# Kernel tuning notes

Measured on AMD Instinct MI355X. Metric: run time of the kernel, lower is better.

The kernel has to match this reference:

```python
import jax, jax.numpy as jnp
import numpy as np

B, T, F, H = 8, 1024, 512, 8
DK = F // H
P = 2 * T - 1  # relative position length


def setup_inputs() -> dict:
    key = jax.random.key(0)
    ks = jax.random.split(key, 16)
    s = 0.02
    inp = {
        "query": jax.random.normal(ks[0], (B, T, F), jnp.float32),
        "key": jax.random.normal(ks[1], (B, T, F), jnp.float32),
        "value": jax.random.normal(ks[2], (B, T, F), jnp.float32),
        "mask": jax.random.randint(ks[3], (B, T, T), 0, 2) > 0,
        "pos_emb": jax.random.normal(ks[4], (1, P, F), jnp.float32),
        "Wq": jax.random.normal(ks[5], (F, F), jnp.float32) * s,
        "bq": jnp.zeros((F,), jnp.float32),
        "Wk": jax.random.normal(ks[6], (F, F), jnp.float32) * s,
        "bk": jnp.zeros((F,), jnp.float32),
        "Wv": jax.random.normal(ks[7], (F, F), jnp.float32) * s,
        "bv": jnp.zeros((F,), jnp.float32),
        "Wpos": jax.random.normal(ks[8], (F, F), jnp.float32) * s,
        "Wo": jax.random.normal(ks[9], (F, F), jnp.float32) * s,
        "bo": jnp.zeros((F,), jnp.float32),
        "pos_bias_u": jax.random.normal(ks[10], (H, DK), jnp.float32) * s,
        "pos_bias_v": jax.random.normal(ks[11], (H, DK), jnp.float32) * s,
    }
    return inp


def _rel_shift(x):
    # x: (b, h, q, p) with p = 2q-1 ; Transformer-XL pad/reshape/slice trick
    b, h, q, p = x.shape
    x = jnp.pad(x, ((0, 0), (0, 0), (0, 0), (1, 0)))
    x = x.reshape(b, h, p + 1, q)[:, :, 1:, :].reshape(b, h, q, p)
    return x


def reference(query, key, value, mask, pos_emb, Wq, bq, Wk, bk, Wv, bv,
              Wpos, Wo, bo, pos_bias_u, pos_bias_v):
    b = query.shape[0]
    # projections (torch Linear: y = x @ W.T + b), split into heads -> (b,h,t,d)
    q = (query @ Wq.T + bq).reshape(b, -1, H, DK).transpose(0, 2, 1, 3)
    k = (key @ Wk.T + bk).reshape(b, -1, H, DK).transpose(0, 2, 1, 3)
    v = (value @ Wv.T + bv).reshape(b, -1, H, DK).transpose(0, 2, 1, 3)
    # positional projection: (1,P,F) -> (h,P,d)
    p = (pos_emb @ Wpos.T).reshape(-1, H, DK).transpose(1, 0, 2)

    q_u = q + pos_bias_u[None, :, None, :]
    q_v = q + pos_bias_v[None, :, None, :]

    matrix_ac = jnp.einsum("bhqd,bhkd->bhqk", q_u, k)
    matrix_bd = jnp.einsum("bhqd,hpd->bhqp", q_v, p)
    matrix_bd = _rel_shift(matrix_bd)[:, :, :, : matrix_ac.shape[-1]]

    scores = (matrix_ac + matrix_bd) / jnp.sqrt(jnp.float32(DK))
    m = mask[:, None, :, :]
    scores = jnp.where(m, -10000.0, scores)
    attn = jax.nn.softmax(scores, axis=-1)
    attn = jnp.where(m, 0.0, attn)

    x = jnp.einsum("bhqk,bhkd->bhqd", attn, v)
    x = x.transpose(0, 2, 1, 3).reshape(b, -1, H * DK)
    return x @ Wo.T + bo
```

## Files before the change

kernel.cpp:

```cpp
#include <hip/hip_runtime.h>

#define Bn 8
#define Tn 1024
#define Fn 512
#define Hn 8
#define DKn 64
#define Pn 2047

namespace {

typedef _Float16 h8 __attribute__((ext_vector_type(8)));
typedef float f4 __attribute__((ext_vector_type(4)));

__device__ __forceinline__ unsigned short f2h(float f) {
  _Float16 h = (_Float16)f;
  return __builtin_bit_cast(unsigned short, h);
}

__device__ __forceinline__ f4 mfma16(h8 a, h8 b, f4 c) {
  return __builtin_amdgcn_mfma_f32_16x16x32_f16(a, b, c, 0, 0, 0);
}

__device__ __forceinline__ h8 frag_ld(const unsigned char* p, int row, int kk, int grp) {
  int off = row * 128 + kk * 64 + grp * 16;
  off ^= (row & 7) << 4;
  return *(const h8*)(p + off);
}

__global__ void detect_kernel(const unsigned int* m, int* flag) {
  if (threadIdx.x == 0) {
    int bm = 0;
    for (int i = 0; i < 256; ++i)
      if (m[i] > 1u) bm = 1;
    *flag = bm;
  }
}

template <int MODE>
__global__ __launch_bounds__(256) void proj_kernel(
    const float* __restrict__ Af, const unsigned short* __restrict__ Ah,
    const float* __restrict__ W, const float* __restrict__ bias,
    const float* __restrict__ pbu, const float* __restrict__ pbv,
    unsigned short* __restrict__ o0, unsigned short* __restrict__ o1,
    float* __restrict__ ofp, int M) {
  __shared__ __align__(16) unsigned char sA[64 * 128];
  __shared__ __align__(16) unsigned char sB[64 * 128];

  const int t = threadIdx.x;
  const int w = t >> 6, l = t & 63;
  const int grp = l >> 4, lc = l & 15;
  const int m0 = blockIdx.x * 64, n0 = blockIdx.y * 64;
  const int srow = t >> 2, sseg = t & 3;

  f4 acc[4];
#pragma unroll
  for (int c = 0; c < 4; ++c) acc[c] = {0.f, 0.f, 0.f, 0.f};

  for (int kt = 0; kt < 8; ++kt) {
    {
      int gm = m0 + srow;
      int sw = (srow & 7) << 4;
      if (MODE == 4) {
        const unsigned short* ar = Ah + (size_t)gm * Fn + kt * 64 + sseg * 16;
#pragma unroll
        for (int hh = 0; hh < 2; ++hh) {
          uint4 qd = *(const uint4*)(ar + hh * 8);
          int off = srow * 128 + sseg * 32 + hh * 16;
          *(uint2*)(sA + ((off) ^ sw)) = make_uint2(qd.x, qd.y);
          *(uint2*)(sA + ((off + 8) ^ sw)) = make_uint2(qd.z, qd.w);
        }
      } else {
        bool valid = (gm < M);
        const float* ar = Af + (size_t)gm * Fn + kt * 64 + sseg * 16;
#pragma unroll
        for (int i = 0; i < 4; ++i) {
          float4 fv = valid ? *(const float4*)(ar + 4 * i) : make_float4(0.f, 0.f, 0.f, 0.f);
          uint2 pk;
          pk.x = (unsigned)f2h(fv.x) | ((unsigned)f2h(fv.y) << 16);
          pk.y = (unsigned)f2h(fv.z) | ((unsigned)f2h(fv.w) << 16);
          int off = srow * 128 + sseg * 32 + i * 8;
          *(uint2*)(sA + (off ^ sw)) = pk;
        }
      }
      const float* br = W + (size_t)(n0 + srow) * Fn + kt * 64 + sseg * 16;
#pragma unroll
      for (int i = 0; i < 4; ++i) {
        float4 fv = *(const float4*)(br + 4 * i);
        uint2 pk;
        pk.x = (unsigned)f2h(fv.x) | ((unsigned)f2h(fv.y) << 16);
        pk.y = (unsigned)f2h(fv.z) | ((unsigned)f2h(fv.w) << 16);
        int off = srow * 128 + sseg * 32 + i * 8;
        *(uint2*)(sB + (off ^ sw)) = pk;
      }
    }
    __syncthreads();
    const int arow = 16 * w + lc;
    h8 a0 = frag_ld(sA, arow, 0, grp);
    h8 a1 = frag_ld(sA, arow, 1, grp);
#pragma unroll
    for (int c = 0; c < 4; ++c) {
      int brow = 16 * c + lc;
      acc[c] = mfma16(a0, frag_ld(sB, brow, 0, grp), acc[c]);
      acc[c] = mfma16(a1, frag_ld(sB, brow, 1, grp), acc[c]);
    }
    __syncthreads();
  }

#pragma unroll
  for (int c = 0; c < 4; ++c) {
#pragma unroll
    for (int r = 0; r < 4; ++r) {
      int m = m0 + 16 * w + grp * 4 + r;
      int n = n0 + 16 * c + lc;
      float vv = acc[c][r];
      if (MODE == 0) {
        vv += bias[n];
        int b = m >> 10, tt = m & 1023, h = n >> 6, d = n & 63;
        size_t qi = ((size_t)(b * Hn + h) * Tn + tt) * DKn + d;
        o0[qi] = f2h(vv + pbu[n]);
        o1[qi] = f2h(vv + pbv[n]);
      } else if (MODE == 1) {
        vv += bias[n];
        int b = m >> 10, tt = m & 1023, h = n >> 6, d = n & 63;
        o0[((size_t)(b * Hn + h) * Tn + tt) * DKn + d] = f2h(vv);
      } else if (MODE == 2) {
        vv += bias[n];
        int b = m >> 10, tt = m & 1023, h = n >> 6, d = n & 63;
        o0[((size_t)(b * Hn + h) * DKn + d) * Tn + tt] = f2h(vv);
      } else if (MODE == 3) {
        if (m < M) {
          int h = n >> 6, d = n & 63;
          o0[((size_t)h * Pn + m) * DKn + d] = f2h(vv);
        }
      } else {
        ofp[(size_t)m * Fn + n] = vv + bias[n];
      }
    }
  }
}

__global__ __launch_bounds__(256) void attn_kernel(
    const unsigned short* __restrict__ Qu, const unsigned short* __restrict__ Qv,
    const unsigned short* __restrict__ Kb, const unsigned short* __restrict__ Vt,
    const unsigned short* __restrict__ Pb, const void* __restrict__ maskp,
    const int* __restrict__ flagp, unsigned short* __restrict__ xb) {
  __shared__ __align__(16) unsigned char sK[64 * 128];
  __shared__ __align__(16) unsigned char sV[64 * 128];
  __shared__ __align__(16) unsigned char sP[128 * 128];
  __shared__ __align__(16) unsigned char sM[64 * 64];
  __shared__ float sBD[64 * 129];
  __shared__ __align__(16) unsigned char sPp[64 * 128];

  const int t = threadIdx.x;
  const int w = t >> 6, l = t & 63;
  const int grp = l >> 4, lc = l & 15;
  const int q0 = blockIdx.x * 64;
  const int bh = blockIdx.y;
  const int b = bh >> 3, h = bh & 7;
  const int byte_mode = *flagp;

  h8 au[2], av[2];
  {
    const size_t qbase = ((size_t)bh * Tn + q0 + 16 * w + lc) * DKn;
#pragma unroll
    for (int kk = 0; kk < 2; ++kk) {
      au[kk] = *(const h8*)(Qu + qbase + kk * 32 + grp * 8);
      av[kk] = *(const h8*)(Qv + qbase + kk * 32 + grp * 8);
    }
  }

  float m_run[4], l_run[4];
  f4 oacc[4];
#pragma unroll
  for (int r = 0; r < 4; ++r) { m_run[r] = -1e30f; l_run[r] = 0.f; }
#pragma unroll
  for (int c = 0; c < 4; ++c) oacc[c] = {0.f, 0.f, 0.f, 0.f};

  const size_t kvbase = (size_t)bh * Tn * DKn;

  for (int kt = 0; kt < 16; ++kt) {
    const int k0 = kt * 64;
    const int pbase = k0 - q0 + 960;

    __syncthreads();
    {
      int row = t >> 2, seg = t & 3;
      int sw = (row & 7) << 4;
      {
        const unsigned short* src = Kb + kvbase + (size_t)(k0 + row) * DKn + seg * 16;
#pragma unroll
        for (int hh = 0; hh < 2; ++hh) {
          uint4 qd = *(const uint4*)(src + hh * 8);
          int off = row * 128 + seg * 32 + hh * 16;
          *(uint2*)(sK + ((off) ^ sw)) = make_uint2(qd.x, qd.y);
          *(uint2*)(sK + ((off + 8) ^ sw)) = make_uint2(qd.z, qd.w);
        }
      }
      {
        const unsigned short* src = Vt + kvbase + (size_t)row * Tn + k0 + seg * 16;
#pragma unroll
        for (int hh = 0; hh < 2; ++hh) {
          uint4 qd = *(const uint4*)(src + hh * 8);
          int off = row * 128 + seg * 32 + hh * 16;
          *(uint2*)(sV + ((off) ^ sw)) = make_uint2(qd.x, qd.y);
          *(uint2*)(sV + ((off + 8) ^ sw)) = make_uint2(qd.z, qd.w);
        }
      }
      if (byte_mode) {
        const unsigned char* mb = (const unsigned char*)maskp + (size_t)b * Tn * Tn +
                                  (size_t)(q0 + row) * Tn + k0 + seg * 16;
        *(uint4*)(sM + row * 64 + seg * 16) = *(const uint4*)mb;
      } else {
        const int* mi = (const int*)maskp + (size_t)b * Tn * Tn + (size_t)(q0 + row) * Tn + k0 + seg * 16;
#pragma unroll
        for (int i2 = 0; i2 < 4; ++i2) {
          int4 qd = *(const int4*)(mi + 4 * i2);
          unsigned pk = (qd.x != 0 ? 1u : 0u) | (qd.y != 0 ? 0x100u : 0u) |
                        (qd.z != 0 ? 0x10000u : 0u) | (qd.w != 0 ? 0x1000000u : 0u);
          *(unsigned*)(sM + row * 64 + seg * 16 + 4 * i2) = pk;
        }
      }
      {
        int prow = t >> 1, pseg = t & 1;
        int gp = pbase + prow;
        if (gp > Pn - 1) gp = Pn - 1;
        const unsigned short* src = Pb + ((size_t)h * Pn + gp) * DKn + pseg * 32;
        int psw = (prow & 7) << 4;
#pragma unroll
        for (int i2 = 0; i2 < 4; ++i2) {
          uint4 qd = *(const uint4*)(src + i2 * 8);
          int off = prow * 128 + pseg * 64 + i2 * 16;
          *(uint2*)(sP + ((off) ^ psw)) = make_uint2(qd.x, qd.y);
          *(uint2*)(sP + ((off + 8) ^ psw)) = make_uint2(qd.z, qd.w);
        }
      }
    }
    __syncthreads();

    f4 ac[4];
#pragma unroll
    for (int c = 0; c < 4; ++c) {
      ac[c] = {0.f, 0.f, 0.f, 0.f};
      int brow = 16 * c + lc;
      ac[c] = mfma16(au[0], frag_ld(sK, brow, 0, grp), ac[c]);
      ac[c] = mfma16(au[1], frag_ld(sK, brow, 1, grp), ac[c]);
    }
#pragma unroll
    for (int c = 0; c < 8; ++c) {
      f4 z = {0.f, 0.f, 0.f, 0.f};
      int brow = 16 * c + lc;
      z = mfma16(av[0], frag_ld(sP, brow, 0, grp), z);
      z = mfma16(av[1], frag_ld(sP, brow, 1, grp), z);
#pragma unroll
      for (int r = 0; r < 4; ++r)
        sBD[(16 * w + grp * 4 + r) * 129 + 16 * c + lc] = z[r];
    }
    __syncthreads();

#pragma unroll
    for (int r = 0; r < 4; ++r) {
      const int row = 16 * w + grp * 4 + r;
      float sc[4];
      bool mk[4];
#pragma unroll
      for (int c = 0; c < 4; ++c) {
        int col = 16 * c + lc;
        float vv = (ac[c][r] + sBD[row * 128 + col + 63]) * 0.125f;
        mk[c] = sM[row * 64 + col] != 0;
        sc[c] = mk[c] ? -10000.f : vv;
      }
      float mx = fmaxf(fmaxf(sc[0], sc[1]), fmaxf(sc[2], sc[3]));
#pragma unroll
      for (int d2 = 1; d2 < 16; d2 <<= 1) mx = fmaxf(mx, __shfl_xor(mx, d2, 64));
      float mnew = fmaxf(m_run[r], mx);
      float scl = __expf(m_run[r] - mnew);
      float ps = 0.f;
      unsigned short ph[4];
#pragma unroll
      for (int c = 0; c < 4; ++c) {
        float p = __expf(sc[c] - mnew);
        ps += p;
        ph[c] = f2h(mk[c] ? 0.f : p);
      }
#pragma unroll
      for (int d2 = 1; d2 < 16; d2 <<= 1) ps += __shfl_xor(ps, d2, 64);
      l_run[r] = l_run[r] * scl + ps;
      m_run[r] = mnew;
#pragma unroll
      for (int c = 0; c < 4; ++c) oacc[c][r] *= scl;
      int sw = (row & 7) << 4;
#pragma unroll
      for (int c = 0; c < 4; ++c) {
        int off = row * 128 + (16 * c + lc) * 2;
        *(unsigned short*)(sPp + (off ^ sw)) = ph[c];
      }
    }
    __syncthreads();

    {
      const int prow_a = 16 * w + lc;
      h8 pa0 = frag_ld(sPp, prow_a, 0, grp);
      h8 pa1 = frag_ld(sPp, prow_a, 1, grp);
#pragma unroll
      for (int c = 0; c < 4; ++c) {
        int brow = 16 * c + lc;
        oacc[c] = mfma16(pa0, frag_ld(sV, brow, 0, grp), oacc[c]);
        oacc[c] = mfma16(pa1, frag_ld(sV, brow, 1, grp), oacc[c]);
      }
    }
  }

#pragma unroll
  for (int c = 0; c < 4; ++c) {
#pragma unroll
    for (int r = 0; r < 4; ++r) {
      int rowq = 16 * w + grp * 4 + r;
      float vv = oacc[c][r] / l_run[r];
      size_t idx = ((size_t)b * Tn + q0 + rowq) * Fn + h * DKn + 16 * c + lc;
      xb[idx] = f2h(vv);
    }
  }
}

}

extern "C" void kernel_launch(void* const* d_in, const int* in_sizes, int n_in,
                              void* d_out, int out_size, void* d_ws, size_t ws_size,
                              hipStream_t stream) {
  const float* query = (const float*)d_in[0];
  const float* key = (const float*)d_in[1];
  const float* value = (const float*)d_in[2];
  const void* maskp = d_in[3];
  const float* pos = (const float*)d_in[4];
  const float* Wq = (const float*)d_in[5];
  const float* bq = (const float*)d_in[6];
  const float* Wk = (const float*)d_in[7];
  const float* bk = (const float*)d_in[8];
  const float* Wv = (const float*)d_in[9];
  const float* bv = (const float*)d_in[10];
  const float* Wpos = (const float*)d_in[11];
  const float* Wo = (const float*)d_in[12];
  const float* bo = (const float*)d_in[13];
  const float* pu = (const float*)d_in[14];
  const float* pv = (const float*)d_in[15];
  float* out = (float*)d_out;

  unsigned char* ws = (unsigned char*)d_ws;
  int* flag = (int*)ws;
  const size_t nQKV = (size_t)Bn * Hn * Tn * DKn;
  const size_t nP = (size_t)Hn * Pn * DKn;
  unsigned short* Qu = (unsigned short*)(ws + 256);
  unsigned short* Qv = Qu + nQKV;
  unsigned short* Kb = Qv + nQKV;
  unsigned short* Vt = Kb + nQKV;
  unsigned short* Pbuf = Vt + nQKV;
  unsigned short* xb = Pbuf + nP;

  detect_kernel<<<dim3(1), dim3(64), 0, stream>>>((const unsigned int*)maskp, flag);
  proj_kernel<0><<<dim3(128, 8), dim3(256), 0, stream>>>(query, nullptr, Wq, bq, pu, pv, Qu, Qv, nullptr, Bn * Tn);
  proj_kernel<1><<<dim3(128, 8), dim3(256), 0, stream>>>(key, nullptr, Wk, bk, nullptr, nullptr, Kb, nullptr, nullptr, Bn * Tn);
  proj_kernel<2><<<dim3(128, 8), dim3(256), 0, stream>>>(value, nullptr, Wv, bv, nullptr, nullptr, Vt, nullptr, nullptr, Bn * Tn);
  proj_kernel<3><<<dim3(32, 8), dim3(256), 0, stream>>>(pos, nullptr, Wpos, nullptr, nullptr, nullptr, Pbuf, nullptr, nullptr, Pn);
  attn_kernel<<<dim3(16, 64), dim3(256), 0, stream>>>(Qu, Qv, Kb, Vt, Pbuf, maskp, flag, xb);
  proj_kernel<4><<<dim3(128, 8), dim3(256), 0, stream>>>(nullptr, xb, Wo, bo, nullptr, nullptr, nullptr, nullptr, out, Bn * Tn);
}
```

Measured before the change: 228.3 us.

## Restructure attention to per-wave smem-free loop and merge QKV/pos projections

The four Q/K/V/pos projection launches are merged into one grid using a z-dimension mode. The attention kernel drops the block-wide shared K/V/P tiles and their barriers. Each wave now reads K, V and positional fragments straight from global memory and keeps only small private buffers for the BD band (stored as fp16), the mask and the P tile. The PV matmul is delayed by one iteration so it overlaps the next tile's mask and score work. Softmax switches to exp2 with the scale folded in, and the launch bound allows three blocks per CU. In exchange, global/L2 traffic goes up because K/V reuse across waves is lost, and storing BD in fp16 costs some precision.

Result: slower. 414.7 us (+81.6%).

```diff
diff --git a/kernel.cpp b/kernel.cpp
--- a/kernel.cpp
+++ b/kernel.cpp
@@ -16,6 +16,9 @@
   _Float16 h = (_Float16)f;
   return __builtin_bit_cast(unsigned short, h);
 }
+__device__ __forceinline__ float h2f(unsigned short u) {
+  return (float)__builtin_bit_cast(_Float16, u);
+}
 
 __device__ __forceinline__ f4 mfma16(h8 a, h8 b, f4 c) {
   return __builtin_amdgcn_mfma_f32_16x16x32_f16(a, b, c, 0, 0, 0);
@@ -36,13 +39,24 @@
   }
 }
 
-template <int MODE>
-__global__ __launch_bounds__(256) void proj_kernel(
-    const float* __restrict__ Af, const unsigned short* __restrict__ Ah,
-    const float* __restrict__ W, const float* __restrict__ bias,
+__global__ __launch_bounds__(256) void qkvp_kernel(
+    const float* __restrict__ Aq, const float* __restrict__ Ak,
+    const float* __restrict__ Av, const float* __restrict__ Ap,
+    const float* __restrict__ Wq, const float* __restrict__ Wk,
+    const float* __restrict__ Wv, const float* __restrict__ Wp,
+    const float* __restrict__ bq, const float* __restrict__ bk,
+    const float* __restrict__ bv,
     const float* __restrict__ pbu, const float* __restrict__ pbv,
-    unsigned short* __restrict__ o0, unsigned short* __restrict__ o1,
-    float* __restrict__ ofp, int M) {
+    unsigned short* __restrict__ Qu, unsigned short* __restrict__ Qv,
+    unsigned short* __restrict__ Kb, unsigned short* __restrict__ Vt,
+    unsigned short* __restrict__ Pbuf) {
+  const int mode = blockIdx.z;
+  if (mode == 3 && blockIdx.x >= 32) return;
+  const float* A = mode == 0 ? Aq : mode == 1 ? Ak : mode == 2 ? Av : Ap;
+  const float* W = mode == 0 ? Wq : mode == 1 ? Wk : mode == 2 ? Wv : Wp;
+  const float* bias = mode == 0 ? bq : mode == 1 ? bk : bv;
+  const int M = mode == 3 ? Pn : Bn * Tn;
+
   __shared__ __align__(16) unsigned char sA[64 * 128];
   __shared__ __align__(16) unsigned char sB[64 * 128];
 
@@ -60,27 +74,16 @@
     {
       int gm = m0 + srow;
       int sw = (srow & 7) << 4;
-      if (MODE == 4) {
-        const unsigned short* ar = Ah + (size_t)gm * Fn + kt * 64 + sseg * 16;
-#pragma unroll
-        for (int hh = 0; hh < 2; ++hh) {
-          uint4 qd = *(const uint4*)(ar + hh * 8);
-          int off = srow * 128 + sseg * 32 + hh * 16;
-          *(uint2*)(sA + ((off) ^ sw)) = make_uint2(qd.x, qd.y);
-          *(uint2*)(sA + ((off + 8) ^ sw)) = make_uint2(qd.z, qd.w);
-        }
-      } else {
-        bool valid = (gm < M);
-        const float* ar = Af + (size_t)gm * Fn + kt * 64 + sseg * 16;
-#pragma unroll
-        for (int i = 0; i < 4; ++i) {
-          float4 fv = valid ? *(const float4*)(ar + 4 * i) : make_float4(0.f, 0.f, 0.f, 0.f);
-          uint2 pk;
-          pk.x = (unsigned)f2h(fv.x) | ((unsigned)f2h(fv.y) << 16);
-          pk.y = (unsigned)f2h(fv.z) | ((unsigned)f2h(fv.w) << 16);
-          int off = srow * 128 + sseg * 32 + i * 8;
-          *(uint2*)(sA + (off ^ sw)) = pk;
-        }
+      bool valid = (gm < M);
+      const float* ar = A + (size_t)gm * Fn + kt * 64 + sseg * 16;
+#pragma unroll
+      for (int i = 0; i < 4; ++i) {
+        float4 fv = valid ? *(const float4*)(ar + 4 * i) : make_float4(0.f, 0.f, 0.f, 0.f);
+        uint2 pk;
+        pk.x = (unsigned)f2h(fv.x) | ((unsigned)f2h(fv.y) << 16);
+        pk.y = (unsigned)f2h(fv.z) | ((unsigned)f2h(fv.w) << 16);
+        int off = srow * 128 + sseg * 32 + i * 8;
+        *(uint2*)(sA + (off ^ sw)) = pk;
       }
       const float* br = W + (size_t)(n0 + srow) * Fn + kt * 64 + sseg * 16;
 #pragma unroll
@@ -113,43 +116,99 @@
       int m = m0 + 16 * w + grp * 4 + r;
       int n = n0 + 16 * c + lc;
       float vv = acc[c][r];
-      if (MODE == 0) {
+      if (mode == 0) {
         vv += bias[n];
         int b = m >> 10, tt = m & 1023, h = n >> 6, d = n & 63;
         size_t qi = ((size_t)(b * Hn + h) * Tn + tt) * DKn + d;
-        o0[qi] = f2h(vv + pbu[n]);
-        o1[qi] = f2h(vv + pbv[n]);
-      } else if (MODE == 1) {
+        Qu[qi] = f2h(vv + pbu[n]);
+        Qv[qi] = f2h(vv + pbv[n]);
+      } else if (mode == 1) {
         vv += bias[n];
         int b = m >> 10, tt = m & 1023, h = n >> 6, d = n & 63;
-        o0[((size_t)(b * Hn + h) * Tn + tt) * DKn + d] = f2h(vv);
-      } else if (MODE == 2) {
+        Kb[((size_t)(b * Hn + h) * Tn + tt) * DKn + d] = f2h(vv);
+      } else if (mode == 2) {
         vv += bias[n];
         int b = m >> 10, tt = m & 1023, h = n >> 6, d = n & 63;
-        o0[((size_t)(b * Hn + h) * DKn + d) * Tn + tt] = f2h(vv);
-      } else if (MODE == 3) {
+        Vt[((size_t)(b * Hn + h) * DKn + d) * Tn + tt] = f2h(vv);
+      } else {
         if (m < M) {
           int h = n >> 6, d = n & 63;
-          o0[((size_t)h * Pn + m) * DKn + d] = f2h(vv);
+          Pbuf[((size_t)h * Pn + m) * DKn + d] = f2h(vv);
         }
-      } else {
-        ofp[(size_t)m * Fn + n] = vv + bias[n];
-      }
-    }
-  }
-}
-
-__global__ __launch_bounds__(256) void attn_kernel(
+      }
+    }
+  }
+}
+
+__global__ __launch_bounds__(256) void oproj_kernel(
+    const unsigned short* __restrict__ Ah, const float* __restrict__ W,
+    const float* __restrict__ bias, float* __restrict__ ofp) {
+  __shared__ __align__(16) unsigned char sA[64 * 128];
+  __shared__ __align__(16) unsigned char sB[64 * 128];
+
+  const int t = threadIdx.x;
+  const int w = t >> 6, l = t & 63;
+  const int grp = l >> 4, lc = l & 15;
+  const int m0 = blockIdx.x * 64, n0 = blockIdx.y * 64;
+  const int srow = t >> 2, sseg = t & 3;
+
+  f4 acc[4];
+#pragma unroll
+  for (int c = 0; c < 4; ++c) acc[c] = {0.f, 0.f, 0.f, 0.f};
+
+  for (int kt = 0; kt < 8; ++kt) {
+    {
+      int gm = m0 + srow;
+      int sw = (srow & 7) << 4;
+      const unsigned short* ar = Ah + (size_t)gm * Fn + kt * 64 + sseg * 16;
+#pragma unroll
+      for (int hh = 0; hh < 2; ++hh) {
+        uint4 qd = *(const uint4*)(ar + hh * 8);
+        int off = srow * 128 + sseg * 32 + hh * 16;
+        *(uint2*)(sA + ((off) ^ sw)) = make_uint2(qd.x, qd.y);
+        *(uint2*)(sA + ((off + 8) ^ sw)) = make_uint2(qd.z, qd.w);
+      }
+      const float* br = W + (size_t)(n0 + srow) * Fn + kt * 64 + sseg * 16;
+#pragma unroll
+      for (int i = 0; i < 4; ++i) {
+        float4 fv = *(const float4*)(br + 4 * i);
+        uint2 pk;
+        pk.x = (unsigned)f2h(fv.x) | ((unsigned)f2h(fv.y) << 16);
+        pk.y = (unsigned)f2h(fv.z) | ((unsigned)f2h(fv.w) << 16);
+        int off = srow * 128 + sseg * 32 + i * 8;
+        *(uint2*)(sB + (off ^ sw)) = pk;
+      }
+    }
+    __syncthreads();
+    const int arow = 16 * w + lc;
+    h8 a0 = frag_ld(sA, arow, 0, grp);
+    h8 a1 = frag_ld(sA, arow, 1, grp);
+#pragma unroll
+    for (int c = 0; c < 4; ++c) {
+      int brow = 16 * c + lc;
+      acc[c] = mfma16(a0, frag_ld(sB, brow, 0, grp), acc[c]);
+      acc[c] = mfma16(a1, frag_ld(sB, brow, 1, grp), acc[c]);
+    }
+    __syncthreads();
+  }
+
+#pragma unroll
+  for (int c = 0; c < 4; ++c) {
+#pragma unroll
+    for (int r = 0; r < 4; ++r) {
+      int m = m0 + 16 * w + grp * 4 + r;
+      int n = n0 + 16 * c + lc;
+      ofp[(size_t)m * Fn + n] = acc[c][r] + bias[n];
+    }
+  }
+}
+
+__global__ __launch_bounds__(256, 3) void attn_kernel(
     const unsigned short* __restrict__ Qu, const unsigned short* __restrict__ Qv,
     const unsigned short* __restrict__ Kb, const unsigned short* __restrict__ Vt,
     const unsigned short* __restrict__ Pb, const void* __restrict__ maskp,
     const int* __restrict__ flagp, unsigned short* __restrict__ xb) {
-  __shared__ __align__(16) unsigned char sK[64 * 128];
-  __shared__ __align__(16) unsigned char sV[64 * 128];
-  __shared__ __align__(16) unsigned char sP[128 * 128];
-  __shared__ __align__(16) unsigned char sM[64 * 64];
-  __shared__ float sBD[64 * 129];
-  __shared__ __align__(16) unsigned char sPp[64 * 128];
+  __shared__ __align__(16) unsigned char smem[4 * 2880 + 4 * 2048 + 4 * 1024];
 
   const int t = threadIdx.x;
   const int w = t >> 6, l = t & 63;
@@ -159,6 +218,10 @@
   const int b = bh >> 3, h = bh & 7;
   const int byte_mode = *flagp;
 
+  unsigned char* bdw = smem + w * 2880;
+  unsigned char* ppw = smem + 11520 + w * 2048;
+  unsigned char* mkw = smem + 19712 + w * 1024;
+
   h8 au[2], av[2];
   {
     const size_t qbase = ((size_t)bh * Tn + q0 + 16 * w + lc) * DKn;
@@ -176,111 +239,89 @@
 #pragma unroll
   for (int c = 0; c < 4; ++c) oacc[c] = {0.f, 0.f, 0.f, 0.f};
 
-  const size_t kvbase = (size_t)bh * Tn * DKn;
+  const unsigned short* Kbh = Kb + (size_t)bh * Tn * DKn;
+  const unsigned short* Vbh = Vt + (size_t)bh * DKn * Tn;
+  const unsigned short* Ph = Pb + (size_t)h * Pn * DKn;
+  const int mrow = l >> 2, mseg = l & 3;
+  const size_t mrowbase = (size_t)b * Tn * Tn + (size_t)(q0 + 16 * w + mrow) * Tn + mseg * 16;
 
   for (int kt = 0; kt < 16; ++kt) {
     const int k0 = kt * 64;
-    const int pbase = k0 - q0 + 960;
-
-    __syncthreads();
-    {
-      int row = t >> 2, seg = t & 3;
-      int sw = (row & 7) << 4;
-      {
-        const unsigned short* src = Kb + kvbase + (size_t)(k0 + row) * DKn + seg * 16;
-#pragma unroll
-        for (int hh = 0; hh < 2; ++hh) {
-          uint4 qd = *(const uint4*)(src + hh * 8);
-          int off = row * 128 + seg * 32 + hh * 16;
-          *(uint2*)(sK + ((off) ^ sw)) = make_uint2(qd.x, qd.y);
-          *(uint2*)(sK + ((off + 8) ^ sw)) = make_uint2(qd.z, qd.w);
-        }
-      }
-      {
-        const unsigned short* src = Vt + kvbase + (size_t)row * Tn + k0 + seg * 16;
-#pragma unroll
-        for (int hh = 0; hh < 2; ++hh) {
-          uint4 qd = *(const uint4*)(src + hh * 8);
-          int off = row * 128 + seg * 32 + hh * 16;
-          *(uint2*)(sV + ((off) ^ sw)) = make_uint2(qd.x, qd.y);
-          *(uint2*)(sV + ((off + 8) ^ sw)) = make_uint2(qd.z, qd.w);
-        }
-      }
-      if (byte_mode) {
-        const unsigned char* mb = (const unsigned char*)maskp + (size_t)b * Tn * Tn +
-                                  (size_t)(q0 + row) * Tn + k0 + seg * 16;
-        *(uint4*)(sM + row * 64 + seg * 16) = *(const uint4*)mb;
-      } else {
-        const int* mi = (const int*)maskp + (size_t)b * Tn * Tn + (size_t)(q0 + row) * Tn + k0 + seg * 16;
-#pragma unroll
-        for (int i2 = 0; i2 < 4; ++i2) {
-          int4 qd = *(const int4*)(mi + 4 * i2);
-          unsigned pk = (qd.x != 0 ? 1u : 0u) | (qd.y != 0 ? 0x100u : 0u) |
-                        (qd.z != 0 ? 0x10000u : 0u) | (qd.w != 0 ? 0x1000000u : 0u);
-          *(unsigned*)(sM + row * 64 + seg * 16 + 4 * i2) = pk;
-        }
-      }
-      {
-        int prow = t >> 1, pseg = t & 1;
-        int gp = pbase + prow;
-        if (gp > Pn - 1) gp = Pn - 1;
-        const unsigned short* src = Pb + ((size_t)h * Pn + gp) * DKn + pseg * 32;
-        int psw = (prow & 7) << 4;
-#pragma unroll
-        for (int i2 = 0; i2 < 4; ++i2) {
-          uint4 qd = *(const uint4*)(src + i2 * 8);
-          int off = prow * 128 + pseg * 64 + i2 * 16;
-          *(uint2*)(sP + ((off) ^ psw)) = make_uint2(qd.x, qd.y);
-          *(uint2*)(sP + ((off + 8) ^ psw)) = make_uint2(qd.z, qd.w);
-        }
-      }
-    }
-    __syncthreads();
+
+    if (byte_mode) {
+      const unsigned char* mb = (const unsigned char*)maskp + mrowbase + k0;
+      *(uint4*)(mkw + mrow * 64 + mseg * 16) = *(const uint4*)mb;
+    } else {
+      const int* mi = (const int*)maskp + mrowbase + k0;
+#pragma unroll
+      for (int i2 = 0; i2 < 4; ++i2) {
+        int4 qd = *(const int4*)(mi + 4 * i2);
+        unsigned pk = (qd.x != 0 ? 1u : 0u) | (qd.y != 0 ? 0x100u : 0u) |
+                      (qd.z != 0 ? 0x10000u : 0u) | (qd.w != 0 ? 0x1000000u : 0u);
+        *(unsigned*)(mkw + mrow * 64 + mseg * 16 + 4 * i2) = pk;
+      }
+    }
+
+    if (kt > 0) {
+      const int kp = k0 - 64;
+      h8 pa0 = frag_ld(ppw, lc, 0, grp);
+      h8 pa1 = frag_ld(ppw, lc, 1, grp);
+#pragma unroll
+      for (int c = 0; c < 4; ++c) {
+        const unsigned short* vr = Vbh + (size_t)(16 * c + lc) * Tn + kp;
+        oacc[c] = mfma16(pa0, *(const h8*)(vr + grp * 8), oacc[c]);
+        oacc[c] = mfma16(pa1, *(const h8*)(vr + 32 + grp * 8), oacc[c]);
+      }
+    }
 
     f4 ac[4];
 #pragma unroll
     for (int c = 0; c < 4; ++c) {
+      const unsigned short* kr = Kbh + (size_t)(k0 + 16 * c + lc) * DKn;
       ac[c] = {0.f, 0.f, 0.f, 0.f};
-      int brow = 16 * c + lc;
-      ac[c] = mfma16(au[0], frag_ld(sK, brow, 0, grp), ac[c]);
-      ac[c] = mfma16(au[1], frag_ld(sK, brow, 1, grp), ac[c]);
-    }
-#pragma unroll
-    for (int c = 0; c < 8; ++c) {
+      ac[c] = mfma16(au[0], *(const h8*)(kr + grp * 8), ac[c]);
+      ac[c] = mfma16(au[1], *(const h8*)(kr + 32 + grp * 8), ac[c]);
+    }
+
+    const int pbase = k0 - q0 - 16 * w + 960;
+#pragma unroll
+    for (int c = 3; c < 8; ++c) {
+      int gp = pbase + 16 * c + lc;
+      if (gp > Pn - 1) gp = Pn - 1;
+      const unsigned short* pr = Ph + (size_t)gp * DKn;
       f4 z = {0.f, 0.f, 0.f, 0.f};
-      int brow = 16 * c + lc;
-      z = mfma16(av[0], frag_ld(sP, brow, 0, grp), z);
-      z = mfma16(av[1], frag_ld(sP, brow, 1, grp), z);
-#pragma unroll
-      for (int r = 0; r < 4; ++r)
-        sBD[(16 * w + grp * 4 + r) * 129 + 16 * c + lc] = z[r];
-    }
-    __syncthreads();
+      z = mfma16(av[0], *(const h8*)(pr + grp * 8), z);
+      z = mfma16(av[1], *(const h8*)(pr + 32 + grp * 8), z);
+      unsigned lo = (unsigned)f2h(z[0]) | ((unsigned)f2h(z[1]) << 16);
+      unsigned hi = (unsigned)f2h(z[2]) | ((unsigned)f2h(z[3]) << 16);
+      unsigned char* dst = bdw + (size_t)((16 * (c - 3) + lc) * 18 + grp * 4) * 2;
+      *(unsigned*)dst = lo;
+      *(unsigned*)(dst + 4) = hi;
+    }
 
 #pragma unroll
     for (int r = 0; r < 4; ++r) {
-      const int row = 16 * w + grp * 4 + r;
+      const int rr = grp * 4 + r;
       float sc[4];
-      bool mk[4];
 #pragma unroll
       for (int c = 0; c < 4; ++c) {
-        int col = 16 * c + lc;
-        float vv = (ac[c][r] + sBD[row * 128 + col + 63]) * 0.125f;
-        mk[c] = sM[row * 64 + col] != 0;
-        sc[c] = mk[c] ? -10000.f : vv;
+        const int col = 16 * c + lc;
+        float bdf = h2f(*(const unsigned short*)(bdw + (size_t)((col - rr + 15) * 18 + rr) * 2));
+        float vv = (ac[c][r] + bdf) * 0.18033688f;
+        sc[c] = mkw[rr * 64 + col] != 0 ? -14427.0f : vv;
       }
       float mx = fmaxf(fmaxf(sc[0], sc[1]), fmaxf(sc[2], sc[3]));
 #pragma unroll
       for (int d2 = 1; d2 < 16; d2 <<= 1) mx = fmaxf(mx, __shfl_xor(mx, d2, 64));
       float mnew = fmaxf(m_run[r], mx);
-      float scl = __expf(m_run[r] - mnew);
+      float scl = exp2f(m_run[r] - mnew);
       float ps = 0.f;
       unsigned short ph[4];
 #pragma unroll
       for (int c = 0; c < 4; ++c) {
-        float p = __expf(sc[c] - mnew);
+        float p = exp2f(sc[c] - mnew);
         ps += p;
-        ph[c] = f2h(mk[c] ? 0.f : p);
+        ph[c] = f2h(p);
       }
 #pragma unroll
       for (int d2 = 1; d2 < 16; d2 <<= 1) ps += __shfl_xor(ps, d2, 64);
@@ -288,25 +329,23 @@
       m_run[r] = mnew;
 #pragma unroll
       for (int c = 0; c < 4; ++c) oacc[c][r] *= scl;
-      int sw = (row & 7) << 4;
+      const int sw = (rr & 7) << 4;
 #pragma unroll
       for (int c = 0; c < 4; ++c) {
-        int off = row * 128 + (16 * c + lc) * 2;
-        *(unsigned short*)(sPp + (off ^ sw)) = ph[c];
-      }
-    }
-    __syncthreads();
-
-    {
-      const int prow_a = 16 * w + lc;
-      h8 pa0 = frag_ld(sPp, prow_a, 0, grp);
-      h8 pa1 = frag_ld(sPp, prow_a, 1, grp);
-#pragma unroll
-      for (int c = 0; c < 4; ++c) {
-        int brow = 16 * c + lc;
-        oacc[c] = mfma16(pa0, frag_ld(sV, brow, 0, grp), oacc[c]);
-        oacc[c] = mfma16(pa1, frag_ld(sV, brow, 1, grp), oacc[c]);
-      }
+        int off = (rr * 128 + (16 * c + lc) * 2) ^ sw;
+        *(unsigned short*)(ppw + off) = ph[c];
+      }
+    }
+  }
+
+  {
+    h8 pa0 = frag_ld(ppw, lc, 0, grp);
+    h8 pa1 = frag_ld(ppw, lc, 1, grp);
+#pragma unroll
+    for (int c = 0; c < 4; ++c) {
+      const unsigned short* vr = Vbh + (size_t)(16 * c + lc) * Tn + 960;
+      oacc[c] = mfma16(pa0, *(const h8*)(vr + grp * 8), oacc[c]);
+      oacc[c] = mfma16(pa1, *(const h8*)(vr + 32 + grp * 8), oacc[c]);
     }
   }
 
@@ -357,10 +396,9 @@
   unsigned short* xb = Pbuf + nP;
 
   detect_kernel<<<dim3(1), dim3(64), 0, stream>>>((const unsigned int*)maskp, flag);
-  proj_kernel<0><<<dim3(128, 8), dim3(256), 0, stream>>>(query, nullptr, Wq, bq, pu, pv, Qu, Qv, nullptr, Bn * Tn);
-  proj_kernel<1><<<dim3(128, 8), dim3(256), 0, stream>>>(key, nullptr, Wk, bk, nullptr, nullptr, Kb, nullptr, nullptr, Bn * Tn);
-  proj_kernel<2><<<dim3(128, 8), dim3(256), 0, stream>>>(value, nullptr, Wv, bv, nullptr, nullptr, Vt, nullptr, nullptr, Bn * Tn);
-  proj_kernel<3><<<dim3(32, 8), dim3(256), 0, stream>>>(pos, nullptr, Wpos, nullptr, nullptr, nullptr, Pbuf, nullptr, nullptr, Pn);
+  qkvp_kernel<<<dim3(128, 8, 4), dim3(256), 0, stream>>>(
+      query, key, value, pos, Wq, Wk, Wv, Wpos, bq, bk, bv, pu, pv,
+      Qu, Qv, Kb, Vt, Pbuf);
   attn_kernel<<<dim3(16, 64), dim3(256), 0, stream>>>(Qu, Qv, Kb, Vt, Pbuf, maskp, flag, xb);
-  proj_kernel<4><<<dim3(128, 8), dim3(256), 0, stream>>>(nullptr, xb, Wo, bo, nullptr, nullptr, nullptr, nullptr, out, Bn * Tn);
-}
+  oproj_kernel<<<dim3(128, 8), dim3(256), 0, stream>>>(xb, Wo, bo, out);
+}
```
